# Kernel optimization log

Hardware: AMD Instinct MI355X
Metric: run time of the kernel (lower is better)

Reference implementation:

```python
import jax, jax.numpy as jnp
import numpy as np

GAMMA = 1.0  # init arg gamma


def setup_inputs() -> dict:
    key = jax.random.key(0)
    ks = jax.random.split(key, 7)
    Bn, C, C_, H = 8, 256, 32, 64
    sc = 1.0 / np.sqrt(C)
    return {
        "x_activation": jax.random.normal(ks[0], (Bn, C, H, H), dtype=jnp.float32),
        "f_w": jax.random.normal(ks[1], (C_, C), dtype=jnp.float32) * sc,
        "f_b": jnp.zeros((C_,), dtype=jnp.float32),
        "g_w": jax.random.normal(ks[2], (C_, C), dtype=jnp.float32) * sc,
        "g_b": jnp.zeros((C_,), dtype=jnp.float32),
        "h_w": jax.random.normal(ks[3], (C, C), dtype=jnp.float32) * sc,
        "h_b": jnp.zeros((C,), dtype=jnp.float32),
    }


def reference(x_activation, f_w, f_b, g_w, g_b, h_w, h_b):
    Bn, C, H, W = x_activation.shape
    N = H * W
    xf = x_activation.reshape(Bn, C, N)  # [B, C, N]
    # 1x1 convs are per-pixel linear maps over channels
    f = jnp.einsum('oc,bcn->bon', f_w, xf) + f_b[:, None]  # [B, C_, N]
    g = jnp.einsum('oc,bcn->bon', g_w, xf) + g_b[:, None]  # [B, C_, N]
    h = jnp.einsum('oc,bcn->bon', h_w, xf) + h_b[:, None]  # [B, C, N]
    # S[b, i, j] = sum_c f[b, c, i] * g[b, c, j]  (f^T @ g), shape [B, N, N]
    S = jnp.einsum('bci,bcj->bij', f, g)
    # NOTE: original uses Softmax(dim=1) -> normalize over the i (query/f) axis
    B = jax.nn.softmax(S, axis=1)
    # O (post-transpose) [b, c, i] = sum_j B[b, i, j] * h[b, c, j]
    O = jnp.einsum('bij,bcj->bci', B, h).reshape(Bn, C, H, W)
    return GAMMA * O + x_activation
```

## Files before the change

### kernel.cpp

```cpp
#include <hip/hip_runtime.h>
#include <hip/hip_fp16.h>
#include <cmath>


#define BN 8
#define CC 256
#define CQ 32
#define NN 4096

typedef _Float16 half8 __attribute__((ext_vector_type(8)));
typedef _Float16 half4v __attribute__((ext_vector_type(4)));
typedef float f32x4 __attribute__((ext_vector_type(4)));

static __device__ __forceinline__ float fexp2(float x) {
    return __builtin_amdgcn_exp2f(x);
}

#define LOG2E 1.44269504f
#define SHIFT2 28.8539008f

__global__ __launch_bounds__(256) void transpose_kernel(
    const float* __restrict__ x, __half* __restrict__ xt,
    const float* __restrict__ fw, const float* __restrict__ gw,
    const float* __restrict__ hw, __half* __restrict__ wf16)
{
    const int gid = blockIdx.x;

    if (gid >= 2048) {
        int i = (gid - 2048) * 256 + threadIdx.x;
        float v;
        if (i < 8192)       v = fw[i];
        else if (i < 16384) v = gw[i - 8192];
        else                v = hw[i - 16384];
        wf16[i] = __float2half(v);
        return;
    }

    const int b = gid & 7, rest = gid >> 3;
    const int n0 = (rest & 63) * 64;
    const int c0 = (rest >> 6) * 64;
    const int tid = threadIdx.x;

    __shared__ float T[64 * 65];

    const float* xb = x + ((size_t)b * CC + c0) * NN + n0;
    const int u  = tid >> 4;
    const int n4 = (tid & 15) * 4;
#pragma unroll
    for (int r = 0; r < 4; ++r) {
        int c = r * 16 + u;
        f32x4 v = __builtin_nontemporal_load((const f32x4*)(xb + (size_t)c * NN + n4));
        T[c * 65 + n4 + 0] = v.x;
        T[c * 65 + n4 + 1] = v.y;
        T[c * 65 + n4 + 2] = v.z;
        T[c * 65 + n4 + 3] = v.w;
    }
    __syncthreads();

    const int lane = tid & 63, w = tid >> 6;
    const int n  = w * 16 + (lane >> 2);
    const int cc = (lane & 3) * 16;
    half8 o0, o1;
#pragma unroll
    for (int k = 0; k < 8; ++k) {
        o0[k] = (_Float16)T[(cc + k) * 65 + n];
        o1[k] = (_Float16)T[(cc + 8 + k) * 65 + n];
    }
    __half* dst = xt + ((size_t)b * NN + n0 + n) * CC + c0 + cc;
    *(half8*)(void*)dst = o0;
    *(half8*)(void*)(dst + 8) = o1;
}

__global__ __launch_bounds__(256) void proj_kernel(
    const __half* __restrict__ xt, const __half* __restrict__ wf16,
    const float* __restrict__ fb, const float* __restrict__ gb,
    const float* __restrict__ hb,
    __half* __restrict__ ft, __half* __restrict__ gt, __half* __restrict__ hm)
{
    const int tid = threadIdx.x;
    const int w = tid >> 6, lane = tid & 63, col = lane & 15, q = lane >> 4;
    const int gid = blockIdx.x;
    const int b = gid & 7, rest = gid >> 3;
    const int n0 = (rest & 63) * 64;
    const int ot = rest >> 6;

    const __half* xtb  = xt + (size_t)b * NN * CC;
    const __half* fw16 = wf16;
    const __half* gw16 = wf16 + 8192;
    const __half* hw16 = wf16 + 16384;

    f32x4 acc[4];
#pragma unroll
    for (int mt = 0; mt < 4; ++mt) acc[mt] = (f32x4){0.f, 0.f, 0.f, 0.f};

    if (ot == 0) {
        const int pix = n0 + 16 * w + col;
#pragma unroll
        for (int ks = 0; ks < 8; ++ks) {
            half8 bf = *(const half8*)(const void*)(xtb + (size_t)pix * CC + ks * 32 + q * 8);
#pragma unroll
            for (int mt = 0; mt < 4; ++mt) {
                const __half* wp = (mt < 2) ? (fw16 + (16 * mt + col) * CC)
                                            : (gw16 + (16 * (mt - 2) + col) * CC);
                half8 af = *(const half8*)(const void*)(wp + ks * 32 + q * 8);
                acc[mt] = __builtin_amdgcn_mfma_f32_16x16x32_f16(af, bf, acc[mt], 0, 0, 0);
            }
        }
#pragma unroll
        for (int mt = 0; mt < 4; ++mt) {
            const int mtl = mt & 1;
            const float* bsel = (mt < 2) ? fb : gb;
            __half* dsel = (mt < 2) ? ft : gt;
            half4v hv;
#pragma unroll
            for (int r = 0; r < 4; ++r)
                hv[r] = (_Float16)(acc[mt][r] + bsel[16 * mtl + 4 * q + r]);
            *(half4v*)(void*)(dsel + ((size_t)b * NN + pix) * CQ + 16 * mtl + 4 * q) = hv;
        }
    } else {
        const int c = (ot - 1) * 64 + 16 * w + col;
#pragma unroll
        for (int ks = 0; ks < 8; ++ks) {
            half8 bf = *(const half8*)(const void*)(hw16 + (size_t)c * CC + ks * 32 + q * 8);
#pragma unroll
            for (int mt = 0; mt < 4; ++mt) {
                half8 af = *(const half8*)(const void*)(xtb + (size_t)(n0 + 16 * mt + col) * CC + ks * 32 + q * 8);
                acc[mt] = __builtin_amdgcn_mfma_f32_16x16x32_f16(af, bf, acc[mt], 0, 0, 0);
            }
        }
        const float bias = hb[c];
#pragma unroll
        for (int mt = 0; mt < 4; ++mt) {
            half4v hv;
#pragma unroll
            for (int r = 0; r < 4; ++r)
                hv[r] = (_Float16)(acc[mt][r] + bias);
            *(half4v*)(void*)(hm + ((size_t)b * CC + c) * NN + n0 + 16 * mt + 4 * q) = hv;
        }
    }
}

__global__ __launch_bounds__(256) void pass1_kernel(
    const __half* __restrict__ ft, const __half* __restrict__ gt,
    float* __restrict__ linv)
{
    const int tid = threadIdx.x;
    const int w = tid >> 6, lane = tid & 63, col = lane & 15, q = lane >> 4;
    const int gid = blockIdx.x;
    const int b = gid & 7;
    const int jg = (gid >> 3) * 64 + 16 * w + col;

    const __half* fbase = ft + (size_t)b * NN * CQ;
    half8 gfrag = *(const half8*)(const void*)(gt + ((size_t)b * NN + jg) * CQ + q * 8);

    float a0 = 0.f, a1 = 0.f, a2 = 0.f, a3 = 0.f;
    const f32x4 zero = {0.f, 0.f, 0.f, 0.f};

    half8 a_cur = *(const half8*)(const void*)(fbase + (size_t)col * CQ + q * 8);
    for (int i0 = 0; i0 < NN; i0 += 16) {
        int i_n = (i0 + 16) & (NN - 1);
        half8 a_next = *(const half8*)(const void*)(fbase + (size_t)(i_n + col) * CQ + q * 8);
        f32x4 d = __builtin_amdgcn_mfma_f32_16x16x32_f16(a_cur, gfrag, zero, 0, 0, 0);
        a0 += fexp2(fmaf(d[0], LOG2E, -SHIFT2));
        a1 += fexp2(fmaf(d[1], LOG2E, -SHIFT2));
        a2 += fexp2(fmaf(d[2], LOG2E, -SHIFT2));
        a3 += fexp2(fmaf(d[3], LOG2E, -SHIFT2));
        a_cur = a_next;
    }
    float l = (a0 + a1) + (a2 + a3);
    l += __shfl_xor(l, 16);
    l += __shfl_xor(l, 32);
    if (q == 0)
        linv[(size_t)b * NN + jg] = 1.f / l;
}

__global__ __launch_bounds__(256, 2) void pass2_kernel(
    const float* __restrict__ x,
    const __half* __restrict__ ft, const __half* __restrict__ gt,
    const __half* __restrict__ hm, const float* __restrict__ linv,
    float* __restrict__ out)
{
    const int tid = threadIdx.x;
    const int w = tid >> 6, lane = tid & 63, col = lane & 15, q = lane >> 4;
    const int gid = blockIdx.x;
    const int b  = gid & 7;
    const int i0 = (gid >> 3) * 64;
    const int cb = 64 * w;

    __shared__ __half P[2][64 * 64];

    const __half* gbase = gt + (size_t)b * NN * CQ;
    const __half* hbase = hm + (size_t)b * CC * NN;
    const float*  lb    = linv + (size_t)b * NN;

    half8 ffr[4];
#pragma unroll
    for (int it = 0; it < 4; ++it)
        ffr[it] = *(const half8*)(const void*)(ft + ((size_t)b * NN + i0 + 16 * it + col) * CQ + q * 8);

    f32x4 acc[4][4];
#pragma unroll
    for (int ms = 0; ms < 4; ++ms)
#pragma unroll
        for (int ns = 0; ns < 4; ++ns)
            acc[ms][ns] = (f32x4){0.f, 0.f, 0.f, 0.f};

    const f32x4 zero = {0.f, 0.f, 0.f, 0.f};
    const int jml = 16 * w + 4 * q;
    const int sw  = 8 * (col & 7);

    half8  gfr = *(const half8*)(const void*)(gbase + (size_t)(16 * w + col) * CQ + q * 8);
    float4 il  = *(const float4*)(lb + jml);

    int buf = 0;
    for (int j0 = 0; j0 < NN; j0 += 64, buf ^= 1) {
        half8 hv[4][2];
#pragma unroll
        for (int ns = 0; ns < 4; ++ns)
#pragma unroll
            for (int ks = 0; ks < 2; ++ks)
                hv[ns][ks] = *(const half8*)(const void*)(
                    hbase + (size_t)(cb + 16 * ns + col) * NN + j0 + ks * 32 + q * 8);

        f32x4 d[4];
#pragma unroll
        for (int it = 0; it < 4; ++it)
            d[it] = __builtin_amdgcn_mfma_f32_16x16x32_f16(gfr, ffr[it], zero, 0, 0, 0);

        const int jn = (j0 + 64) & (NN - 1);
        half8  gfr_n = *(const half8*)(const void*)(gbase + (size_t)(jn + 16 * w + col) * CQ + q * 8);
        float4 il_n  = *(const float4*)(lb + jn + jml);

        __half* Pb = &P[buf][0];
#pragma unroll
        for (int it = 0; it < 4; ++it) {
            half4v pv;
            pv[0] = (_Float16)(fexp2(fmaf(d[it][0], LOG2E, -SHIFT2)) * il.x);
            pv[1] = (_Float16)(fexp2(fmaf(d[it][1], LOG2E, -SHIFT2)) * il.y);
            pv[2] = (_Float16)(fexp2(fmaf(d[it][2], LOG2E, -SHIFT2)) * il.z);
            pv[3] = (_Float16)(fexp2(fmaf(d[it][3], LOG2E, -SHIFT2)) * il.w);
            *(half4v*)(void*)(Pb + (16 * it + col) * 64 + (jml ^ sw)) = pv;
        }
        __syncthreads();

#pragma unroll
        for (int ks = 0; ks < 2; ++ks) {
            half8 af[4];
#pragma unroll
            for (int ms = 0; ms < 4; ++ms)
                af[ms] = *(const half8*)(const void*)(
                    Pb + (16 * ms + col) * 64 + ((ks * 32 + q * 8) ^ sw));
#pragma unroll
            for (int ms = 0; ms < 4; ++ms)
#pragma unroll
                for (int ns = 0; ns < 4; ++ns)
                    acc[ms][ns] = __builtin_amdgcn_mfma_f32_16x16x32_f16(
                        af[ms], hv[ns][ks], acc[ms][ns], 0, 0, 0);
        }
        gfr = gfr_n;
        il  = il_n;
    }

    const float* xb = x + (size_t)b * CC * NN;
    float* ob = out + (size_t)b * CC * NN;
#pragma unroll
    for (int ms = 0; ms < 4; ++ms) {
#pragma unroll
        for (int ns = 0; ns < 4; ++ns) {
            int c  = cb + 16 * ns + col;
            int ii = i0 + 16 * ms + 4 * q;
            size_t off = (size_t)c * NN + ii;
            f32x4 xv = __builtin_nontemporal_load((const f32x4*)(xb + off));
            f32x4 ov;
            ov.x = acc[ms][ns][0] + xv.x;
            ov.y = acc[ms][ns][1] + xv.y;
            ov.z = acc[ms][ns][2] + xv.z;
            ov.w = acc[ms][ns][3] + xv.w;
            __builtin_nontemporal_store(ov, (f32x4*)(ob + off));
        }
    }
}

extern "C" void kernel_launch(void* const* d_in, const int* in_sizes, int n_in,
                              void* d_out, int out_size, void* d_ws, size_t ws_size,
                              hipStream_t stream)
{
    const float* x  = (const float*)d_in[0];
    const float* fw = (const float*)d_in[1];
    const float* fb = (const float*)d_in[2];
    const float* gw = (const float*)d_in[3];
    const float* gb = (const float*)d_in[4];
    const float* hw = (const float*)d_in[5];
    const float* hb = (const float*)d_in[6];
    float* out = (float*)d_out;

    char* ws = (char*)d_ws;
    __half* xt = (__half*)(ws);
    __half* wf = (__half*)(ws + (size_t)16777216);
    __half* ft = (__half*)(ws + (size_t)17039360);
    __half* gt = (__half*)(ws + (size_t)19136512);
    __half* hm = (__half*)(ws + (size_t)21233664);
    float*  lv = (float*) (ws + (size_t)38010880);

    transpose_kernel<<<dim3(2368), dim3(256), 0, stream>>>(x, xt, fw, gw, hw, wf);
    proj_kernel<<<dim3(2560), dim3(256), 0, stream>>>(xt, wf, fb, gb, hb, ft, gt, hm);
    pass1_kernel<<<dim3(512), dim3(256), 0, stream>>>(ft, gt, lv);
    pass2_kernel<<<dim3(512), dim3(256), 0, stream>>>(x, ft, gt, hm, lv, out);
}
```

Measured before the change: 326.2 us.

## Keep softmax probabilities in registers, drop LDS round-trip and barrier in pass2

Pass2 now has each wave compute the full 64x64 score tile itself, four MFMAs per 16-column slice. The MFMA output layout is fed directly as the A operand of a 16x16x16 MFMA against h, so the shared-memory P buffer and the per-iteration __syncthreads go away. Pass1 now stores -log2(l)-shift, so normalisation folds into the exp2 FMA and the separate multiply is gone. The cost is four times the S MFMAs per wave, half-K MFMAs for the PV product, and more registers for prefetched g and h fragments.

```diff
diff --git a/kernel.cpp b/kernel.cpp
--- a/kernel.cpp
+++ b/kernel.cpp
@@ -142,7 +142,7 @@
 
 __global__ __launch_bounds__(256) void pass1_kernel(
     const __half* __restrict__ ft, const __half* __restrict__ gt,
-    float* __restrict__ linv)
+    float* __restrict__ shl)
 {
     const int tid = threadIdx.x;
     const int w = tid >> 6, lane = tid & 63, col = lane & 15, q = lane >> 4;
@@ -171,13 +171,13 @@
     l += __shfl_xor(l, 16);
     l += __shfl_xor(l, 32);
     if (q == 0)
-        linv[(size_t)b * NN + jg] = 1.f / l;
+        shl[(size_t)b * NN + jg] = -__log2f(l) - SHIFT2;
 }
 
 __global__ __launch_bounds__(256, 2) void pass2_kernel(
     const float* __restrict__ x,
     const __half* __restrict__ ft, const __half* __restrict__ gt,
-    const __half* __restrict__ hm, const float* __restrict__ linv,
+    const __half* __restrict__ hm, const float* __restrict__ shl,
     float* __restrict__ out)
 {
     const int tid = threadIdx.x;
@@ -187,95 +187,101 @@
     const int i0 = (gid >> 3) * 64;
     const int cb = 64 * w;
 
-    __shared__ __half P[2][64 * 64];
-
     const __half* gbase = gt + (size_t)b * NN * CQ;
     const __half* hbase = hm + (size_t)b * CC * NN;
-    const float*  lb    = linv + (size_t)b * NN;
+    const float*  lb    = shl + (size_t)b * NN;
 
     half8 ffr[4];
 #pragma unroll
     for (int it = 0; it < 4; ++it)
         ffr[it] = *(const half8*)(const void*)(ft + ((size_t)b * NN + i0 + 16 * it + col) * CQ + q * 8);
 
+    const __half* hrow[4];
+#pragma unroll
+    for (int ns = 0; ns < 4; ++ns)
+        hrow[ns] = hbase + (size_t)(cb + 16 * ns + col) * NN + 4 * q;
+
     f32x4 acc[4][4];
 #pragma unroll
-    for (int ms = 0; ms < 4; ++ms)
+    for (int it = 0; it < 4; ++it)
 #pragma unroll
         for (int ns = 0; ns < 4; ++ns)
-            acc[ms][ns] = (f32x4){0.f, 0.f, 0.f, 0.f};
+            acc[it][ns] = (f32x4){0.f, 0.f, 0.f, 0.f};
 
     const f32x4 zero = {0.f, 0.f, 0.f, 0.f};
-    const int jml = 16 * w + 4 * q;
-    const int sw  = 8 * (col & 7);
-
-    half8  gfr = *(const half8*)(const void*)(gbase + (size_t)(16 * w + col) * CQ + q * 8);
-    float4 il  = *(const float4*)(lb + jml);
-
-    int buf = 0;
-    for (int j0 = 0; j0 < NN; j0 += 64, buf ^= 1) {
-        half8 hv[4][2];
+
+    half8 gfr[4], gfr_n[4];
+#pragma unroll
+    for (int jt = 0; jt < 4; ++jt)
+        gfr[jt] = *(const half8*)(const void*)(gbase + (size_t)(16 * jt + col) * CQ + q * 8);
+    half4v hv[4][4], hv_n[4][4];
+#pragma unroll
+    for (int ns = 0; ns < 4; ++ns)
+#pragma unroll
+        for (int jt = 0; jt < 4; ++jt)
+            hv[ns][jt] = *(const half4v*)(const void*)(hrow[ns] + 16 * jt);
+
+    for (int j0 = 0; j0 < NN; j0 += 64) {
+        const int jn = (j0 + 64) & (NN - 1);
+#pragma unroll
+        for (int jt = 0; jt < 4; ++jt) {
+            f32x4 sl = *(const f32x4*)(lb + j0 + 16 * jt + 4 * q);
+
+            f32x4 d[4];
+#pragma unroll
+            for (int it = 0; it < 4; ++it)
+                d[it] = __builtin_amdgcn_mfma_f32_16x16x32_f16(gfr[jt], ffr[it], zero, 0, 0, 0);
+
+            if (jt == 0) {
+#pragma unroll
+                for (int k = 0; k < 4; ++k)
+                    gfr_n[k] = *(const half8*)(const void*)(gbase + (size_t)(jn + 16 * k + col) * CQ + q * 8);
+            }
+            if (jt == 1) {
+#pragma unroll
+                for (int ns = 0; ns < 4; ++ns)
+#pragma unroll
+                    for (int k = 0; k < 4; ++k)
+                        hv_n[ns][k] = *(const half4v*)(const void*)(hrow[ns] + jn + 16 * k);
+            }
+
+            half4v pa[4];
+#pragma unroll
+            for (int it = 0; it < 4; ++it)
+#pragma unroll
+                for (int r = 0; r < 4; ++r)
+                    pa[it][r] = (_Float16)fexp2(fmaf(d[it][r], LOG2E, sl[r]));
+
+#pragma unroll
+            for (int it = 0; it < 4; ++it)
+#pragma unroll
+                for (int ns = 0; ns < 4; ++ns)
+                    acc[it][ns] = __builtin_amdgcn_mfma_f32_16x16x16f16(
+                        pa[it], hv[ns][jt], acc[it][ns], 0, 0, 0);
+        }
+#pragma unroll
+        for (int k = 0; k < 4; ++k) gfr[k] = gfr_n[k];
 #pragma unroll
         for (int ns = 0; ns < 4; ++ns)
 #pragma unroll
-            for (int ks = 0; ks < 2; ++ks)
-                hv[ns][ks] = *(const half8*)(const void*)(
-                    hbase + (size_t)(cb + 16 * ns + col) * NN + j0 + ks * 32 + q * 8);
-
-        f32x4 d[4];
-#pragma unroll
-        for (int it = 0; it < 4; ++it)
-            d[it] = __builtin_amdgcn_mfma_f32_16x16x32_f16(gfr, ffr[it], zero, 0, 0, 0);
-
-        const int jn = (j0 + 64) & (NN - 1);
-        half8  gfr_n = *(const half8*)(const void*)(gbase + (size_t)(jn + 16 * w + col) * CQ + q * 8);
-        float4 il_n  = *(const float4*)(lb + jn + jml);
-
-        __half* Pb = &P[buf][0];
-#pragma unroll
-        for (int it = 0; it < 4; ++it) {
-            half4v pv;
-            pv[0] = (_Float16)(fexp2(fmaf(d[it][0], LOG2E, -SHIFT2)) * il.x);
-            pv[1] = (_Float16)(fexp2(fmaf(d[it][1], LOG2E, -SHIFT2)) * il.y);
-            pv[2] = (_Float16)(fexp2(fmaf(d[it][2], LOG2E, -SHIFT2)) * il.z);
-            pv[3] = (_Float16)(fexp2(fmaf(d[it][3], LOG2E, -SHIFT2)) * il.w);
-            *(half4v*)(void*)(Pb + (16 * it + col) * 64 + (jml ^ sw)) = pv;
-        }
-        __syncthreads();
-
-#pragma unroll
-        for (int ks = 0; ks < 2; ++ks) {
-            half8 af[4];
-#pragma unroll
-            for (int ms = 0; ms < 4; ++ms)
-                af[ms] = *(const half8*)(const void*)(
-                    Pb + (16 * ms + col) * 64 + ((ks * 32 + q * 8) ^ sw));
-#pragma unroll
-            for (int ms = 0; ms < 4; ++ms)
-#pragma unroll
-                for (int ns = 0; ns < 4; ++ns)
-                    acc[ms][ns] = __builtin_amdgcn_mfma_f32_16x16x32_f16(
-                        af[ms], hv[ns][ks], acc[ms][ns], 0, 0, 0);
-        }
-        gfr = gfr_n;
-        il  = il_n;
+            for (int k = 0; k < 4; ++k) hv[ns][k] = hv_n[ns][k];
     }
 
     const float* xb = x + (size_t)b * CC * NN;
     float* ob = out + (size_t)b * CC * NN;
 #pragma unroll
-    for (int ms = 0; ms < 4; ++ms) {
+    for (int it = 0; it < 4; ++it) {
 #pragma unroll
         for (int ns = 0; ns < 4; ++ns) {
             int c  = cb + 16 * ns + col;
-            int ii = i0 + 16 * ms + 4 * q;
+            int ii = i0 + 16 * it + 4 * q;
             size_t off = (size_t)c * NN + ii;
             f32x4 xv = __builtin_nontemporal_load((const f32x4*)(xb + off));
             f32x4 ov;
-            ov.x = acc[ms][ns][0] + xv.x;
-            ov.y = acc[ms][ns][1] + xv.y;
-            ov.z = acc[ms][ns][2] + xv.z;
-            ov.w = acc[ms][ns][3] + xv.w;
+            ov.x = acc[it][ns][0] + xv.x;
+            ov.y = acc[it][ns][1] + xv.y;
+            ov.z = acc[it][ns][2] + xv.z;
+            ov.w = acc[it][ns][3] + xv.w;
             __builtin_nontemporal_store(ov, (f32x4*)(ob + off));
         }
     }
```

After: 472.4 us. +44.8%, slower.

## Fuse transpose into projection via LDS tile, fold softmax normalizer into exponent

Applied to the files above, without the earlier changes.

Merges the transpose and projection kernels so each block transposes a 64-pixel x 256-channel tile of x into swizzled LDS and computes the f, g and h projections from it. This removes the fp16 xt round trip through global memory and one launch. Pass1 now handles two MFMA tiles per iteration and stores -log2(l)-shift instead of 1/l, so pass2 adds the normalizer inside the exp2 argument rather than multiplying after it. The fused kernel uses more LDS and registers and launches fewer blocks (512 instead of 2560), which may reduce occupancy.

```diff
diff --git a/kernel.cpp b/kernel.cpp
--- a/kernel.cpp
+++ b/kernel.cpp
@@ -19,60 +19,20 @@
 #define LOG2E 1.44269504f
 #define SHIFT2 28.8539008f
 
-__global__ __launch_bounds__(256) void transpose_kernel(
-    const float* __restrict__ x, __half* __restrict__ xt,
+__global__ __launch_bounds__(256) void cvtw_kernel(
     const float* __restrict__ fw, const float* __restrict__ gw,
     const float* __restrict__ hw, __half* __restrict__ wf16)
 {
-    const int gid = blockIdx.x;
-
-    if (gid >= 2048) {
-        int i = (gid - 2048) * 256 + threadIdx.x;
-        float v;
-        if (i < 8192)       v = fw[i];
-        else if (i < 16384) v = gw[i - 8192];
-        else                v = hw[i - 16384];
-        wf16[i] = __float2half(v);
-        return;
-    }
-
-    const int b = gid & 7, rest = gid >> 3;
-    const int n0 = (rest & 63) * 64;
-    const int c0 = (rest >> 6) * 64;
-    const int tid = threadIdx.x;
-
-    __shared__ float T[64 * 65];
-
-    const float* xb = x + ((size_t)b * CC + c0) * NN + n0;
-    const int u  = tid >> 4;
-    const int n4 = (tid & 15) * 4;
-#pragma unroll
-    for (int r = 0; r < 4; ++r) {
-        int c = r * 16 + u;
-        f32x4 v = __builtin_nontemporal_load((const f32x4*)(xb + (size_t)c * NN + n4));
-        T[c * 65 + n4 + 0] = v.x;
-        T[c * 65 + n4 + 1] = v.y;
-        T[c * 65 + n4 + 2] = v.z;
-        T[c * 65 + n4 + 3] = v.w;
-    }
-    __syncthreads();
-
-    const int lane = tid & 63, w = tid >> 6;
-    const int n  = w * 16 + (lane >> 2);
-    const int cc = (lane & 3) * 16;
-    half8 o0, o1;
-#pragma unroll
-    for (int k = 0; k < 8; ++k) {
-        o0[k] = (_Float16)T[(cc + k) * 65 + n];
-        o1[k] = (_Float16)T[(cc + 8 + k) * 65 + n];
-    }
-    __half* dst = xt + ((size_t)b * NN + n0 + n) * CC + c0 + cc;
-    *(half8*)(void*)dst = o0;
-    *(half8*)(void*)(dst + 8) = o1;
-}
-
-__global__ __launch_bounds__(256) void proj_kernel(
-    const __half* __restrict__ xt, const __half* __restrict__ wf16,
+    int i = blockIdx.x * 256 + threadIdx.x;
+    float v;
+    if (i < 8192)       v = fw[i];
+    else if (i < 16384) v = gw[i - 8192];
+    else                v = hw[i - 16384];
+    wf16[i] = __float2half(v);
+}
+
+__global__ __launch_bounds__(256) void tp_proj_kernel(
+    const float* __restrict__ x, const __half* __restrict__ wf16,
     const float* __restrict__ fb, const float* __restrict__ gb,
     const float* __restrict__ hb,
     __half* __restrict__ ft, __half* __restrict__ gt, __half* __restrict__ hm)
@@ -80,24 +40,55 @@
     const int tid = threadIdx.x;
     const int w = tid >> 6, lane = tid & 63, col = lane & 15, q = lane >> 4;
     const int gid = blockIdx.x;
-    const int b = gid & 7, rest = gid >> 3;
-    const int n0 = (rest & 63) * 64;
-    const int ot = rest >> 6;
-
-    const __half* xtb  = xt + (size_t)b * NN * CC;
-    const __half* fw16 = wf16;
-    const __half* gw16 = wf16 + 8192;
-    const __half* hw16 = wf16 + 16384;
-
-    f32x4 acc[4];
-#pragma unroll
-    for (int mt = 0; mt < 4; ++mt) acc[mt] = (f32x4){0.f, 0.f, 0.f, 0.f};
-
-    if (ot == 0) {
-        const int pix = n0 + 16 * w + col;
+    const int b  = gid & 7;
+    const int n0 = (gid >> 3) * 64;
+
+    __shared__ float  T[64 * 65];
+    __shared__ __half XT[64 * 256];
+
+    const int u  = tid >> 4;
+    const int n4 = (tid & 15) * 4;
+    const int nn = w * 16 + (lane >> 2);
+    const int cc = (lane & 3) * 16;
+    const int sA = 8 * (nn & 7);
+    for (int c4 = 0; c4 < 4; ++c4) {
+        const int c0 = c4 * 64;
+        const float* xb = x + ((size_t)b * CC + c0) * NN + n0;
+#pragma unroll
+        for (int r = 0; r < 4; ++r) {
+            int c = r * 16 + u;
+            f32x4 v = __builtin_nontemporal_load((const f32x4*)(xb + (size_t)c * NN + n4));
+            T[c * 65 + n4 + 0] = v.x;
+            T[c * 65 + n4 + 1] = v.y;
+            T[c * 65 + n4 + 2] = v.z;
+            T[c * 65 + n4 + 3] = v.w;
+        }
+        __syncthreads();
+        half8 o0, o1;
+#pragma unroll
+        for (int k = 0; k < 8; ++k) {
+            o0[k] = (_Float16)T[(cc + k) * 65 + nn];
+            o1[k] = (_Float16)T[(cc + 8 + k) * 65 + nn];
+        }
+        *(half8*)(void*)(&XT[nn * 256 + ((c0 + cc) ^ sA)])     = o0;
+        *(half8*)(void*)(&XT[nn * 256 + ((c0 + cc + 8) ^ sA)]) = o1;
+        __syncthreads();
+    }
+
+    const f32x4 zero = {0.f, 0.f, 0.f, 0.f};
+    const int sw = 8 * (col & 7);
+
+    {
+        const __half* fw16 = wf16;
+        const __half* gw16 = wf16 + 8192;
+        f32x4 acc[4];
+#pragma unroll
+        for (int mt = 0; mt < 4; ++mt) acc[mt] = zero;
+        const int pixl = 16 * w + col;
 #pragma unroll
         for (int ks = 0; ks < 8; ++ks) {
-            half8 bf = *(const half8*)(const void*)(xtb + (size_t)pix * CC + ks * 32 + q * 8);
+            half8 bf = *(const half8*)(const void*)(
+                &XT[pixl * 256 + ((ks * 32 + q * 8) ^ sw)]);
 #pragma unroll
             for (int mt = 0; mt < 4; ++mt) {
                 const __half* wp = (mt < 2) ? (fw16 + (16 * mt + col) * CC)
@@ -106,6 +97,7 @@
                 acc[mt] = __builtin_amdgcn_mfma_f32_16x16x32_f16(af, bf, acc[mt], 0, 0, 0);
             }
         }
+        const int pix = n0 + pixl;
 #pragma unroll
         for (int mt = 0; mt < 4; ++mt) {
             const int mtl = mt & 1;
@@ -117,32 +109,52 @@
                 hv[r] = (_Float16)(acc[mt][r] + bsel[16 * mtl + 4 * q + r]);
             *(half4v*)(void*)(dsel + ((size_t)b * NN + pix) * CQ + 16 * mtl + 4 * q) = hv;
         }
-    } else {
-        const int c = (ot - 1) * 64 + 16 * w + col;
+    }
+
+    {
+        const __half* hw16 = wf16 + 16384;
+        f32x4 acc[4][4];
+#pragma unroll
+        for (int mt = 0; mt < 4; ++mt)
+#pragma unroll
+            for (int ci = 0; ci < 4; ++ci) acc[mt][ci] = zero;
 #pragma unroll
         for (int ks = 0; ks < 8; ++ks) {
-            half8 bf = *(const half8*)(const void*)(hw16 + (size_t)c * CC + ks * 32 + q * 8);
+            half8 af[4], bf[4];
+#pragma unroll
+            for (int mt = 0; mt < 4; ++mt)
+                af[mt] = *(const half8*)(const void*)(
+                    &XT[(16 * mt + col) * 256 + ((ks * 32 + q * 8) ^ sw)]);
+#pragma unroll
+            for (int ci = 0; ci < 4; ++ci)
+                bf[ci] = *(const half8*)(const void*)(
+                    hw16 + (size_t)(16 * (4 * w + ci) + col) * CC + ks * 32 + q * 8);
+#pragma unroll
+            for (int mt = 0; mt < 4; ++mt)
+#pragma unroll
+                for (int ci = 0; ci < 4; ++ci)
+                    acc[mt][ci] = __builtin_amdgcn_mfma_f32_16x16x32_f16(
+                        af[mt], bf[ci], acc[mt][ci], 0, 0, 0);
+        }
+#pragma unroll
+        for (int ci = 0; ci < 4; ++ci) {
+            const int c = 16 * (4 * w + ci) + col;
+            const float bias = hb[c];
 #pragma unroll
             for (int mt = 0; mt < 4; ++mt) {
-                half8 af = *(const half8*)(const void*)(xtb + (size_t)(n0 + 16 * mt + col) * CC + ks * 32 + q * 8);
-                acc[mt] = __builtin_amdgcn_mfma_f32_16x16x32_f16(af, bf, acc[mt], 0, 0, 0);
+                half4v hv;
+#pragma unroll
+                for (int r = 0; r < 4; ++r)
+                    hv[r] = (_Float16)(acc[mt][ci][r] + bias);
+                *(half4v*)(void*)(hm + ((size_t)b * CC + c) * NN + n0 + 16 * mt + 4 * q) = hv;
             }
-        }
-        const float bias = hb[c];
-#pragma unroll
-        for (int mt = 0; mt < 4; ++mt) {
-            half4v hv;
-#pragma unroll
-            for (int r = 0; r < 4; ++r)
-                hv[r] = (_Float16)(acc[mt][r] + bias);
-            *(half4v*)(void*)(hm + ((size_t)b * CC + c) * NN + n0 + 16 * mt + 4 * q) = hv;
         }
     }
 }
 
 __global__ __launch_bounds__(256) void pass1_kernel(
     const __half* __restrict__ ft, const __half* __restrict__ gt,
-    float* __restrict__ linv)
+    float* __restrict__ shl)
 {
     const int tid = threadIdx.x;
     const int w = tid >> 6, lane = tid & 63, col = lane & 15, q = lane >> 4;
@@ -156,28 +168,32 @@
     float a0 = 0.f, a1 = 0.f, a2 = 0.f, a3 = 0.f;
     const f32x4 zero = {0.f, 0.f, 0.f, 0.f};
 
-    half8 a_cur = *(const half8*)(const void*)(fbase + (size_t)col * CQ + q * 8);
-    for (int i0 = 0; i0 < NN; i0 += 16) {
-        int i_n = (i0 + 16) & (NN - 1);
-        half8 a_next = *(const half8*)(const void*)(fbase + (size_t)(i_n + col) * CQ + q * 8);
-        f32x4 d = __builtin_amdgcn_mfma_f32_16x16x32_f16(a_cur, gfrag, zero, 0, 0, 0);
-        a0 += fexp2(fmaf(d[0], LOG2E, -SHIFT2));
-        a1 += fexp2(fmaf(d[1], LOG2E, -SHIFT2));
-        a2 += fexp2(fmaf(d[2], LOG2E, -SHIFT2));
-        a3 += fexp2(fmaf(d[3], LOG2E, -SHIFT2));
-        a_cur = a_next;
+    half8 a0v = *(const half8*)(const void*)(fbase + (size_t)col * CQ + q * 8);
+    half8 a1v = *(const half8*)(const void*)(fbase + (size_t)(16 + col) * CQ + q * 8);
+    for (int i0 = 0; i0 < NN; i0 += 32) {
+        int i_n = (i0 + 32) & (NN - 1);
+        half8 a2v = *(const half8*)(const void*)(fbase + (size_t)(i_n + col) * CQ + q * 8);
+        half8 a3v = *(const half8*)(const void*)(fbase + (size_t)(i_n + 16 + col) * CQ + q * 8);
+        f32x4 d0 = __builtin_amdgcn_mfma_f32_16x16x32_f16(a0v, gfrag, zero, 0, 0, 0);
+        f32x4 d1 = __builtin_amdgcn_mfma_f32_16x16x32_f16(a1v, gfrag, zero, 0, 0, 0);
+        a0 += fexp2(fmaf(d0[0], LOG2E, -SHIFT2)) + fexp2(fmaf(d1[0], LOG2E, -SHIFT2));
+        a1 += fexp2(fmaf(d0[1], LOG2E, -SHIFT2)) + fexp2(fmaf(d1[1], LOG2E, -SHIFT2));
+        a2 += fexp2(fmaf(d0[2], LOG2E, -SHIFT2)) + fexp2(fmaf(d1[2], LOG2E, -SHIFT2));
+        a3 += fexp2(fmaf(d0[3], LOG2E, -SHIFT2)) + fexp2(fmaf(d1[3], LOG2E, -SHIFT2));
+        a0v = a2v;
+        a1v = a3v;
     }
     float l = (a0 + a1) + (a2 + a3);
     l += __shfl_xor(l, 16);
     l += __shfl_xor(l, 32);
     if (q == 0)
-        linv[(size_t)b * NN + jg] = 1.f / l;
+        shl[(size_t)b * NN + jg] = -__log2f(l) - SHIFT2;
 }
 
 __global__ __launch_bounds__(256, 2) void pass2_kernel(
     const float* __restrict__ x,
     const __half* __restrict__ ft, const __half* __restrict__ gt,
-    const __half* __restrict__ hm, const float* __restrict__ linv,
+    const __half* __restrict__ hm, const float* __restrict__ shl,
     float* __restrict__ out)
 {
     const int tid = threadIdx.x;
@@ -191,7 +207,7 @@
 
     const __half* gbase = gt + (size_t)b * NN * CQ;
     const __half* hbase = hm + (size_t)b * CC * NN;
-    const float*  lb    = linv + (size_t)b * NN;
+    const float*  lb    = shl + (size_t)b * NN;
 
     half8 ffr[4];
 #pragma unroll
@@ -209,8 +225,8 @@
     const int jml = 16 * w + 4 * q;
     const int sw  = 8 * (col & 7);
 
-    half8  gfr = *(const half8*)(const void*)(gbase + (size_t)(16 * w + col) * CQ + q * 8);
-    float4 il  = *(const float4*)(lb + jml);
+    half8 gfr = *(const half8*)(const void*)(gbase + (size_t)(16 * w + col) * CQ + q * 8);
+    f32x4 sl  = *(const f32x4*)(lb + jml);
 
     int buf = 0;
     for (int j0 = 0; j0 < NN; j0 += 64, buf ^= 1) {
@@ -228,17 +244,17 @@
             d[it] = __builtin_amdgcn_mfma_f32_16x16x32_f16(gfr, ffr[it], zero, 0, 0, 0);
 
         const int jn = (j0 + 64) & (NN - 1);
-        half8  gfr_n = *(const half8*)(const void*)(gbase + (size_t)(jn + 16 * w + col) * CQ + q * 8);
-        float4 il_n  = *(const float4*)(lb + jn + jml);
+        half8 gfr_n = *(const half8*)(const void*)(gbase + (size_t)(jn + 16 * w + col) * CQ + q * 8);
+        f32x4 sl_n  = *(const f32x4*)(lb + jn + jml);
 
         __half* Pb = &P[buf][0];
 #pragma unroll
         for (int it = 0; it < 4; ++it) {
             half4v pv;
-            pv[0] = (_Float16)(fexp2(fmaf(d[it][0], LOG2E, -SHIFT2)) * il.x);
-            pv[1] = (_Float16)(fexp2(fmaf(d[it][1], LOG2E, -SHIFT2)) * il.y);
-            pv[2] = (_Float16)(fexp2(fmaf(d[it][2], LOG2E, -SHIFT2)) * il.z);
-            pv[3] = (_Float16)(fexp2(fmaf(d[it][3], LOG2E, -SHIFT2)) * il.w);
+            pv[0] = (_Float16)fexp2(fmaf(d[it][0], LOG2E, sl[0]));
+            pv[1] = (_Float16)fexp2(fmaf(d[it][1], LOG2E, sl[1]));
+            pv[2] = (_Float16)fexp2(fmaf(d[it][2], LOG2E, sl[2]));
+            pv[3] = (_Float16)fexp2(fmaf(d[it][3], LOG2E, sl[3]));
             *(half4v*)(void*)(Pb + (16 * it + col) * 64 + (jml ^ sw)) = pv;
         }
         __syncthreads();
@@ -258,7 +274,7 @@
                         af[ms], hv[ns][ks], acc[ms][ns], 0, 0, 0);
         }
         gfr = gfr_n;
-        il  = il_n;
+        sl  = sl_n;
     }
 
     const float* xb = x + (size_t)b * CC * NN;
@@ -295,15 +311,14 @@
     float* out = (float*)d_out;
 
     char* ws = (char*)d_ws;
-    __half* xt = (__half*)(ws);
-    __half* wf = (__half*)(ws + (size_t)16777216);
-    __half* ft = (__half*)(ws + (size_t)17039360);
-    __half* gt = (__half*)(ws + (size_t)19136512);
-    __half* hm = (__half*)(ws + (size_t)21233664);
-    float*  lv = (float*) (ws + (size_t)38010880);
-
-    transpose_kernel<<<dim3(2368), dim3(256), 0, stream>>>(x, xt, fw, gw, hw, wf);
-    proj_kernel<<<dim3(2560), dim3(256), 0, stream>>>(xt, wf, fb, gb, hb, ft, gt, hm);
+    __half* wf = (__half*)(ws);
+    __half* ft = (__half*)(ws + (size_t)262144);
+    __half* gt = (__half*)(ws + (size_t)2359296);
+    __half* hm = (__half*)(ws + (size_t)4456448);
+    float*  lv = (float*) (ws + (size_t)21233664);
+
+    cvtw_kernel<<<dim3(320), dim3(256), 0, stream>>>(fw, gw, hw, wf);
+    tp_proj_kernel<<<dim3(512), dim3(256), 0, stream>>>(x, wf, fb, gb, hb, ft, gt, hm);
     pass1_kernel<<<dim3(512), dim3(256), 0, stream>>>(ft, gt, lv);
     pass2_kernel<<<dim3(512), dim3(256), 0, stream>>>(x, ft, gt, hm, lv, out);
 }
```

Result: faster. 294.1 us (-9.9%).
